# Performance work log

Measured on AMD Instinct MI355X. Metric: run time of the kernel, lower is better.

## Reference

```python
import jax, jax.numpy as jnp
import numpy as np

B, L, D, N, H = 4, 1024, 1024, 16, 64  # batch, seq, d_model, n_head, d_head
R = 2 * L  # relative position table length
EPS = 1e-5


def setup_inputs() -> dict:
    key = jax.random.key(0)
    ks = jax.random.split(key, 16)
    s = D ** -0.5
    q = jax.random.normal(ks[0], (B, L, D), jnp.float32)
    k = jax.random.normal(ks[1], (B, L, D), jnp.float32)
    v = jax.random.normal(ks[2], (B, L, D), jnp.float32)
    pos_encodings = jax.random.normal(ks[3], (R, D), jnp.float32)
    padding = jax.random.randint(ks[4], (B, 1, 1, L), 0, 2).astype(bool)
    q_w = jax.random.normal(ks[5], (D, N, H), jnp.float32) * s
    k_w = jax.random.normal(ks[6], (D, N, H), jnp.float32) * s
    k_b = jnp.zeros((N, H), jnp.float32)
    v_w = jax.random.normal(ks[7], (D, N, H), jnp.float32) * s
    v_b = jnp.zeros((N, H), jnp.float32)
    r_w_bias = jax.random.normal(ks[8], (N, 1, H), jnp.float32) * 0.02
    r_r_bias = jax.random.normal(ks[9], (N, 1, H), jnp.float32) * 0.02
    r_kernel = jax.random.normal(ks[10], (N, D, H), jnp.float32) * s
    post_w = jax.random.normal(ks[11], (N, H, D), jnp.float32) * (N * H) ** -0.5
    post_b = jnp.zeros((D,), jnp.float32)
    ln_g = jnp.ones((D,), jnp.float32)
    ln_b = jnp.zeros((D,), jnp.float32)
    return dict(q=q, k=k, v=v, pos_encodings=pos_encodings, padding=padding,
                q_w=q_w, k_w=k_w, k_b=k_b, v_w=v_w, v_b=v_b,
                r_w_bias=r_w_bias, r_r_bias=r_r_bias, r_kernel=r_kernel,
                post_w=post_w, post_b=post_b, ln_g=ln_g, ln_b=ln_b)


def _funnel_attention(q, k, v, pos_encodings, padding, q_w, k_w, k_b, v_w, v_b,
                      r_w_bias, r_r_bias, r_kernel, post_w, post_b, ln_g, ln_b):
    input_q = q
    d_head = q_w.shape[-1]
    scale = d_head ** -0.5
    # head projections, laid out [b, n, l, h]
    qh = jnp.einsum('bld,dnh->bnlh', q, q_w)
    kh = jnp.einsum('bld,dnh->bnlh', k, k_w) + k_b[None, :, None, :]
    vh = jnp.einsum('bld,dnh->bnlh', v, v_w) + v_b[None, :, None, :]
    # content term with r_w_bias
    attn_score = jnp.einsum('bnlh,bnmh->bnlm', qh + r_w_bias[None], kh) * scale
    # relative-position term (rel_shift)
    r = jnp.einsum('rd,ndh->nrh', pos_encodings, r_kernel)  # [n, R, h]
    pos = jnp.einsum('bnlh,nrh->bnlr', qh + r_r_bias[None], r) * scale  # [b,n,L,R]
    b, n, q_len, r_len = pos.shape
    k_len = kh.shape[-2]
    shift = 1 + (q_len != k_len)
    pos = pos.reshape(b, n, r_len, q_len)
    pos = pos[:, :, shift:, :]
    pos = pos.reshape(b, n, q_len, r_len - shift)[..., :k_len]
    attn_score = attn_score + pos
    # key padding mask
    attn_score = attn_score - 1e6 * padding.astype(attn_score.dtype)
    attn_dist = jax.nn.softmax(attn_score, axis=-1)
    out = jnp.einsum('bnlm,bnmh->bnlh', attn_dist, vh)
    attn_out = jnp.einsum('bnlh,nhd->bld', out, post_w) + post_b
    x = input_q + attn_out
    mu = jnp.mean(x, axis=-1, keepdims=True)
    var = jnp.mean(jnp.square(x - mu), axis=-1, keepdims=True)
    return (x - mu) * jax.lax.rsqrt(var + EPS) * ln_g + ln_b


def reference(q, k, v, pos_encodings, padding, q_w, k_w, k_b, v_w, v_b,
              r_w_bias, r_r_bias, r_kernel, post_w, post_b, ln_g, ln_b):
    return _funnel_attention(q, k, v, pos_encodings, padding, q_w, k_w, k_b,
                             v_w, v_b, r_w_bias, r_r_bias, r_kernel,
                             post_w, post_b, ln_g, ln_b)
```

## Files before the change

kernel.cpp:

```cpp
#include <hip/hip_runtime.h>
#include <hip/hip_bf16.h>

#define Bb 4
#define Ls 1024
#define Dd 1024
#define Nn 16
#define Hh 64
#define Rr 2048

typedef __attribute__((ext_vector_type(8))) short short8;
typedef __attribute__((ext_vector_type(4))) short short4v;
typedef __attribute__((ext_vector_type(4))) float f32x4;

__device__ __forceinline__ float bf2f(short s) {
    union { unsigned u; float f; } c;
    c.u = ((unsigned)(unsigned short)s) << 16;
    return c.f;
}
__device__ __forceinline__ short f2bf(float f) {
    __hip_bfloat16 h = __float2bfloat16(f);
    return *reinterpret_cast<short*>(&h);
}

__device__ __forceinline__ void gld16(const void* g, void* l) {
    __builtin_amdgcn_global_load_lds(
        (const __attribute__((address_space(1))) unsigned int*)g,
        (__attribute__((address_space(3))) unsigned int*)l, 16, 0, 0);
}

struct CopyDesc {
    const float* src[4];
    short* dst[4];
    int n[4];
};

__global__ __launch_bounds__(256) void f2bf_multi(CopyDesc cd) {
    const int z = blockIdx.y;
    const int base = (blockIdx.x * 256 + threadIdx.x) * 8;
    if (base >= cd.n[z]) return;
    const float* s = cd.src[z] + base;
    const float4 a = *(const float4*)s;
    const float4 b = *(const float4*)(s + 4);
    short8 o;
    o[0] = f2bf(a.x); o[1] = f2bf(a.y); o[2] = f2bf(a.z); o[3] = f2bf(a.w);
    o[4] = f2bf(b.x); o[5] = f2bf(b.y); o[6] = f2bf(b.z); o[7] = f2bf(b.w);
    *(short8*)(cd.dst[z] + base) = o;
}

struct TransDesc {
    const float* src[4];
    short* dst[4];
};

__global__ __launch_bounds__(256) void transpose_all(
    TransDesc td, const float* __restrict__ rker, short* __restrict__ rkT)
{
    const int z = blockIdx.z;
    const float* in; short* out; int C, R;
    if (z < 4) {
        in = td.src[z]; out = td.dst[z]; C = 1024; R = 1024;
    } else {
        if (blockIdx.x != 0) return;
        in  = rker + (long)(z - 4) * 1024 * 64;
        out = rkT  + (long)(z - 4) * 64 * 1024;
        C = 64; R = 1024;
    }
    const int r0 = blockIdx.y * 64, c0 = blockIdx.x * 64;
    __shared__ float T[64][65];
    const int t = threadIdx.x;
    const int rr = t >> 4, c4 = (t & 15) * 4;
#pragma unroll
    for (int p = 0; p < 4; ++p) {
        const float4 v = *(const float4*)&in[(long)(r0 + p * 16 + rr) * C + c0 + c4];
        T[p * 16 + rr][c4 + 0] = v.x;
        T[p * 16 + rr][c4 + 1] = v.y;
        T[p * 16 + rr][c4 + 2] = v.z;
        T[p * 16 + rr][c4 + 3] = v.w;
    }
    __syncthreads();
#pragma unroll
    for (int p = 0; p < 4; ++p) {
        const int j = p * 16 + (t >> 4);
        const int d4 = (t & 15) * 4;
        short4v o;
#pragma unroll
        for (int u = 0; u < 4; ++u) o[u] = f2bf(T[d4 + u][j]);
        *(short4v*)&out[(long)(c0 + j) * R + r0 + d4] = o;
    }
}

__global__ __launch_bounds__(256) void gemm_bt(
    const short* __restrict__ A, int lda, long aStride,
    const short* __restrict__ Bt, int ldb, long bStride,
    const float* __restrict__ bias,
    const float* __restrict__ kb, const float* __restrict__ vb,
    const float* __restrict__ residual, int ldr,
    void* __restrict__ Cv, int ldc, long cStride, int out_bf16, int K, int y3cut)
{
    const int z = blockIdx.z;
    if (z == 3 && (int)blockIdx.y >= y3cut) return;
    A  += (long)z * aStride;
    Bt += (long)z * bStride;

    const int row0 = blockIdx.y * 128;
    const int col0 = blockIdx.x * 128;

    __shared__ short As[128 * 32];
    __shared__ short Bs[128 * 32];

    const int tid  = threadIdx.x;
    const int w    = tid >> 6;
    const int lane = tid & 63;
    const int quad = lane >> 4;
    const int ln16 = lane & 15;
    const int wr   = (w >> 1) * 64;
    const int wc   = (w & 1) * 64;

    f32x4 acc[4][4];
#pragma unroll
    for (int a = 0; a < 4; ++a)
#pragma unroll
        for (int b = 0; b < 4; ++b) acc[a][b] = (f32x4){0.f, 0.f, 0.f, 0.f};

    const int srow = w * 16 + (lane >> 2);
    const int scol = (lane & 3) * 8;
    const short* gA = A  + (long)(row0 + srow) * lda + scol;
    const short* gB = Bt + (long)(col0 + srow) * ldb + scol;
    short* lA0 = As + w * 512;
    short* lB0 = Bs + w * 512;

    for (int k0 = 0; k0 < K; k0 += 32) {
        __syncthreads();
        gld16(gA + k0,                  lA0);
        gld16(gA + k0 + (long)64 * lda, lA0 + 2048);
        gld16(gB + k0,                  lB0);
        gld16(gB + k0 + (long)64 * ldb, lB0 + 2048);
        __syncthreads();

        short8 af[4], bfr[4];
#pragma unroll
        for (int tm = 0; tm < 4; ++tm)
            af[tm] = *(const short8*)&As[(wr + tm * 16 + ln16) * 32 + quad * 8];
#pragma unroll
        for (int tn = 0; tn < 4; ++tn)
            bfr[tn] = *(const short8*)&Bs[(wc + tn * 16 + ln16) * 32 + quad * 8];
#pragma unroll
        for (int tm = 0; tm < 4; ++tm)
#pragma unroll
            for (int tn = 0; tn < 4; ++tn)
                acc[tm][tn] = __builtin_amdgcn_mfma_f32_16x16x32_bf16(
                    af[tm], bfr[tn], acc[tm][tn], 0, 0, 0);
    }

    const float* bz = bias;
    if (z == 1) bz = kb;
    else if (z == 2) bz = vb;

    float bv[4];
#pragma unroll
    for (int tn = 0; tn < 4; ++tn)
        bv[tn] = bz ? bz[col0 + wc + tn * 16 + ln16] : 0.f;

    short* Cb = (short*)Cv + (long)z * cStride;
    float* Cf = (float*)Cv + (long)z * cStride;
#pragma unroll
    for (int tm = 0; tm < 4; ++tm) {
#pragma unroll
        for (int r = 0; r < 4; ++r) {
            const long row = row0 + wr + tm * 16 + quad * 4 + r;
#pragma unroll
            for (int tn = 0; tn < 4; ++tn) {
                const int col = col0 + wc + tn * 16 + ln16;
                float val = acc[tm][tn][r] + bv[tn];
                if (residual) val += residual[row * (long)ldr + col];
                if (out_bf16) Cb[row * (long)ldc + col] = f2bf(val);
                else          Cf[row * (long)ldc + col] = val;
            }
        }
    }
}

#define SCALE_L2E 0.18033688f

__global__ __launch_bounds__(256, 2) void attn_mfma(
    const short* __restrict__ qh, const short* __restrict__ kh,
    const short* __restrict__ vh, const short* __restrict__ rS,
    const int* __restrict__ padding, const float* __restrict__ rwb,
    const float* __restrict__ rrb, short* __restrict__ ao)
{
    const int lt = blockIdx.x, n = blockIdx.y, b = blockIdx.z;
    const int l0 = lt * 128;
    const int tid  = threadIdx.x;
    const int w    = tid >> 6;
    const int lane = tid & 63;
    const int quad = lane >> 4;
    const int ln16 = lane & 15;
    const int qb   = w * 32;

    __shared__ __align__(16) short ks[64][72];
    __shared__ __align__(16) short vsT[64][72];
    __shared__ __align__(16) short psm[4][16][72];
    __shared__ float padsAll[Ls];

    for (int i = tid; i < Ls; i += 256) {
        const float mask = -1.0e6f * (float)padding[b * Ls + i];
        padsAll[i] = (mask - 16.0f) * 1.44269504f;
    }

    short8 qwf[2][2], qrf[2][2];
#pragma unroll
    for (int qt = 0; qt < 2; ++qt) {
        const long rowoff =
            ((long)(b * Ls + l0 + qb + qt * 16 + ln16)) * (Nn * Hh) + n * Hh;
#pragma unroll
        for (int c = 0; c < 2; ++c) {
            const int kb2 = c * 32 + quad * 8;
            short8 qv = *(const short8*)(qh + rowoff + kb2);
#pragma unroll
            for (int j = 0; j < 8; ++j) {
                float qf = bf2f(qv[j]);
                qwf[qt][c][j] = f2bf(qf + rwb[n * Hh + kb2 + j]);
                qrf[qt][c][j] = f2bf(qf + rrb[n * Hh + kb2 + j]);
            }
        }
    }

    float lsum[2][4];
    f32x4 accO[2][4];
#pragma unroll
    for (int qt = 0; qt < 2; ++qt)
#pragma unroll
        for (int r = 0; r < 4; ++r) {
            lsum[qt][r] = 0.f;
            accO[qt][r] = (f32x4){0.f, 0.f, 0.f, 0.f};
        }

    for (int mt = 0; mt < Ls / 64; ++mt) {
        const int m0 = mt * 64;
        __syncthreads();

#pragma unroll
        for (int p = 0; p < 2; ++p) {
            int idx = tid + p * 256;
            int r_ = idx >> 3, cq = (idx & 7) * 8;
            *(short8*)&ks[r_][cq] =
                *(const short8*)(kh + ((long)(b * Ls + m0 + r_)) * 1024 + n * 64 + cq);
        }
        {
            int kp = tid & 31, cq = (tid >> 5) * 8;
            const short* vp = vh + ((long)(b * Ls + m0 + 2 * kp)) * 1024 + n * 64 + cq;
            short8 va = *(const short8*)vp;
            short8 vb2 = *(const short8*)(vp + 1024);
#pragma unroll
            for (int u = 0; u < 8; ++u) {
                unsigned pk = ((unsigned)(unsigned short)va[u]) |
                              (((unsigned)(unsigned short)vb2[u]) << 16);
                *(unsigned*)&vsT[cq + u][2 * kp] = pk;
            }
        }
        __syncthreads();

        const int baseU = 993 + m0 - l0 - qb;
        short8 rfU[6][2];
#pragma unroll
        for (int s = 0; s < 6; ++s) {
            int row = baseU + s * 16 + ln16;
            row = row < 2047 ? row : 2047;
            const short* rp = rS + (long)row * 1024 + n * 64 + quad * 8;
            rfU[s][0] = *(const short8*)rp;
            rfU[s][1] = *(const short8*)(rp + 32);
        }

#pragma unroll
        for (int qt = 0; qt < 2; ++qt) {
            const int off = qt ? 0 : 1;

            f32x4 Sf[4];
#pragma unroll
            for (int t = 0; t < 4; ++t) {
                f32x4 c = (f32x4){0.f, 0.f, 0.f, 0.f};
#pragma unroll
                for (int c2 = 0; c2 < 2; ++c2) {
                    short8 kf = *(short8*)&ks[t * 16 + ln16][c2 * 32 + quad * 8];
                    c = __builtin_amdgcn_mfma_f32_16x16x32_bf16(qwf[qt][c2], kf, c, 0, 0, 0);
                }
                Sf[t] = c;
            }
            f32x4 Prf[5];
#pragma unroll
            for (int t = 0; t < 5; ++t) {
                f32x4 c = (f32x4){0.f, 0.f, 0.f, 0.f};
                c = __builtin_amdgcn_mfma_f32_16x16x32_bf16(qrf[qt][0], rfU[t + off][0], c, 0, 0, 0);
                c = __builtin_amdgcn_mfma_f32_16x16x32_bf16(qrf[qt][1], rfU[t + off][1], c, 0, 0, 0);
                Prf[t] = c;
            }
            const float mb0 = padsAll[m0 + ln16];
            const float mb1 = padsAll[m0 + 16 + ln16];
            const float mb2 = padsAll[m0 + 32 + ln16];
            const float mb3 = padsAll[m0 + 48 + ln16];
#pragma unroll
            for (int r = 0; r < 4; ++r) {
                const int row = quad * 4 + r;
                const int u = ln16 - row + 15;
                const int srcLane = (quad << 4) | (u & 15);
                const float s0 = __shfl(Prf[0][r], srcLane, 64);
                const float s1 = __shfl(Prf[1][r], srcLane, 64);
                const float s2 = __shfl(Prf[2][r], srcLane, 64);
                const float s3 = __shfl(Prf[3][r], srcLane, 64);
                const float s4 = __shfl(Prf[4][r], srcLane, 64);
                const bool hi = (u >= 16);
                const float p0 = __builtin_amdgcn_exp2f(
                    fmaf(Sf[0][r] + (hi ? s1 : s0), SCALE_L2E, mb0));
                const float p1 = __builtin_amdgcn_exp2f(
                    fmaf(Sf[1][r] + (hi ? s2 : s1), SCALE_L2E, mb1));
                const float p2 = __builtin_amdgcn_exp2f(
                    fmaf(Sf[2][r] + (hi ? s3 : s2), SCALE_L2E, mb2));
                const float p3 = __builtin_amdgcn_exp2f(
                    fmaf(Sf[3][r] + (hi ? s4 : s3), SCALE_L2E, mb3));
                lsum[qt][r] += (p0 + p1) + (p2 + p3);
                psm[w][row][ln16]      = f2bf(p0);
                psm[w][row][16 + ln16] = f2bf(p1);
                psm[w][row][32 + ln16] = f2bf(p2);
                psm[w][row][48 + ln16] = f2bf(p3);
            }

            short8 pA[2];
#pragma unroll
            for (int c2 = 0; c2 < 2; ++c2)
                pA[c2] = *(short8*)&psm[w][ln16][c2 * 32 + quad * 8];
#pragma unroll
            for (int t = 0; t < 4; ++t) {
                f32x4 c = accO[qt][t];
#pragma unroll
                for (int c2 = 0; c2 < 2; ++c2) {
                    short8 vf = *(short8*)&vsT[t * 16 + ln16][c2 * 32 + quad * 8];
                    c = __builtin_amdgcn_mfma_f32_16x16x32_bf16(pA[c2], vf, c, 0, 0, 0);
                }
                accO[qt][t] = c;
            }
        }
    }

#pragma unroll
    for (int qt = 0; qt < 2; ++qt) {
#pragma unroll
        for (int r = 0; r < 4; ++r) {
            float v = lsum[qt][r];
#pragma unroll
            for (int of = 1; of < 16; of <<= 1) v += __shfl_xor(v, of, 64);
            lsum[qt][r] = 1.f / v;
        }
#pragma unroll
        for (int t = 0; t < 4; ++t)
#pragma unroll
            for (int r = 0; r < 4; ++r)
                psm[w][quad * 4 + r][t * 16 + ln16] =
                    f2bf(accO[qt][t][r] * lsum[qt][(unsigned)r]);
#pragma unroll
        for (int p = 0; p < 2; ++p) {
            const int c = lane + p * 64;
            const int row = c >> 3, cq = (c & 7) * 8;
            const long grow = (long)(b * Ls + l0 + qb + qt * 16 + row);
            *(short8*)(ao + grow * 1024 + n * 64 + cq) = *(short8*)&psm[w][row][cq];
        }
    }
}

__global__ __launch_bounds__(256) void ln_kernel(
    float* x, const float* __restrict__ g, const float* __restrict__ bb)
{
    const int row = blockIdx.x;
    const int tid = threadIdx.x;
    float4 v = ((const float4*)(x + (long)row * Dd))[tid];
    float s  = v.x + v.y + v.z + v.w;
    float sq = v.x * v.x + v.y * v.y + v.z * v.z + v.w * v.w;
#pragma unroll
    for (int off = 32; off; off >>= 1) {
        s  += __shfl_down(s, off, 64);
        sq += __shfl_down(sq, off, 64);
    }
    __shared__ float ws_s[4], ws_q[4];
    __shared__ float s_mu, s_rstd;
    const int wave = tid >> 6, lane = tid & 63;
    if (lane == 0) { ws_s[wave] = s; ws_q[wave] = sq; }
    __syncthreads();
    if (tid == 0) {
        const float ts = ws_s[0] + ws_s[1] + ws_s[2] + ws_s[3];
        const float tq = ws_q[0] + ws_q[1] + ws_q[2] + ws_q[3];
        const float mu = ts / (float)Dd;
        const float var = tq / (float)Dd - mu * mu;
        s_mu = mu;
        s_rstd = rsqrtf(var + 1e-5f);
    }
    __syncthreads();
    const float mu = s_mu, rstd = s_rstd;
    const float4 gv = ((const float4*)g)[tid];
    const float4 bv = ((const float4*)bb)[tid];
    float4 o;
    o.x = (v.x - mu) * rstd * gv.x + bv.x;
    o.y = (v.y - mu) * rstd * gv.y + bv.y;
    o.z = (v.z - mu) * rstd * gv.z + bv.z;
    o.w = (v.w - mu) * rstd * gv.w + bv.w;
    ((float4*)(x + (long)row * Dd))[tid] = o;
}

extern "C" void kernel_launch(void* const* d_in, const int* in_sizes, int n_in,
                              void* d_out, int out_size, void* d_ws, size_t ws_size,
                              hipStream_t stream) {
    const float* q      = (const float*)d_in[0];
    const float* k      = (const float*)d_in[1];
    const float* v      = (const float*)d_in[2];
    const float* posenc = (const float*)d_in[3];
    const int*   pad    = (const int*)  d_in[4];
    const float* q_w    = (const float*)d_in[5];
    const float* k_w    = (const float*)d_in[6];
    const float* k_b    = (const float*)d_in[7];
    const float* v_w    = (const float*)d_in[8];
    const float* v_b    = (const float*)d_in[9];
    const float* rwb    = (const float*)d_in[10];
    const float* rrb    = (const float*)d_in[11];
    const float* r_ker  = (const float*)d_in[12];
    const float* post_w = (const float*)d_in[13];
    const float* post_b = (const float*)d_in[14];
    const float* ln_g   = (const float*)d_in[15];
    const float* ln_b   = (const float*)d_in[16];
    float* out = (float*)d_out;

    const long M1 = 1L << 20;
    short* ws = (short*)d_ws;
    short* xq   = ws;
    short* xk   = ws + 4 * M1;
    short* xv   = ws + 8 * M1;
    short* pe   = ws + 12 * M1;
    short* wT   = ws + 14 * M1;
    short* rkT  = ws + 17 * M1;
    short* pwT  = ws + 18 * M1;
    short* qh   = ws + 19 * M1;
    short* kh   = ws + 23 * M1;
    short* vh   = ws + 27 * M1;
    short* rS   = ws + 31 * M1;
    short* ao   = xq;

    const dim3 blk(256);

    CopyDesc cd;
    cd.src[0] = q;      cd.dst[0] = xq;  cd.n[0] = 4 * (int)M1;
    cd.src[1] = k;      cd.dst[1] = xk;  cd.n[1] = 4 * (int)M1;
    cd.src[2] = v;      cd.dst[2] = xv;  cd.n[2] = 4 * (int)M1;
    cd.src[3] = posenc; cd.dst[3] = pe;  cd.n[3] = 2 * (int)M1;
    f2bf_multi<<<dim3(2048, 4), blk, 0, stream>>>(cd);

    TransDesc td;
    td.src[0] = q_w;    td.dst[0] = wT;
    td.src[1] = k_w;    td.dst[1] = wT + M1;
    td.src[2] = v_w;    td.dst[2] = wT + 2 * M1;
    td.src[3] = post_w; td.dst[3] = pwT;
    transpose_all<<<dim3(16, 16, 20), blk, 0, stream>>>(td, r_ker, rkT);

    gemm_bt<<<dim3(8, 32, 4), blk, 0, stream>>>(
        xq, 1024, 4 * M1, wT, 1024, M1, nullptr, k_b, v_b,
        nullptr, 0, qh, 1024, 4 * M1, 1, 1024, 16);

    attn_mfma<<<dim3(Ls / 128, Nn, Bb), blk, 0, stream>>>(
        qh, kh, vh, rS, pad, rwb, rrb, ao);

    gemm_bt<<<dim3(8, 32, 1), blk, 0, stream>>>(
        ao, 1024, 0, pwT, 1024, 0, post_b, nullptr, nullptr,
        q, 1024, out, 1024, 0, 0, 1024, 9999);

    ln_kernel<<<dim3(Bb * Ls), blk, 0, stream>>>(out, ln_g, ln_b);
}
```

Before: 333.9 us.

## Use 8 waves per attention block with one 16-row query tile each

```diff
diff --git a/kernel.cpp b/kernel.cpp
--- a/kernel.cpp
+++ b/kernel.cpp
@@ -182,7 +182,7 @@
 
 #define SCALE_L2E 0.18033688f
 
-__global__ __launch_bounds__(256, 2) void attn_mfma(
+__global__ __launch_bounds__(512, 4) void attn_mfma(
     const short* __restrict__ qh, const short* __restrict__ kh,
     const short* __restrict__ vh, const short* __restrict__ rS,
     const int* __restrict__ padding, const float* __restrict__ rwb,
@@ -195,23 +195,22 @@
     const int lane = tid & 63;
     const int quad = lane >> 4;
     const int ln16 = lane & 15;
-    const int qb   = w * 32;
+    const int qb   = w * 16;
 
     __shared__ __align__(16) short ks[64][72];
     __shared__ __align__(16) short vsT[64][72];
-    __shared__ __align__(16) short psm[4][16][72];
+    __shared__ __align__(16) short psm[8][16][72];
     __shared__ float padsAll[Ls];
 
-    for (int i = tid; i < Ls; i += 256) {
+    for (int i = tid; i < Ls; i += 512) {
         const float mask = -1.0e6f * (float)padding[b * Ls + i];
         padsAll[i] = (mask - 16.0f) * 1.44269504f;
     }
 
-    short8 qwf[2][2], qrf[2][2];
-#pragma unroll
-    for (int qt = 0; qt < 2; ++qt) {
+    short8 qwf[2], qrf[2];
+    {
         const long rowoff =
-            ((long)(b * Ls + l0 + qb + qt * 16 + ln16)) * (Nn * Hh) + n * Hh;
+            ((long)(b * Ls + l0 + qb + ln16)) * (Nn * Hh) + n * Hh;
 #pragma unroll
         for (int c = 0; c < 2; ++c) {
             const int kb2 = c * 32 + quad * 8;
@@ -219,150 +218,138 @@
 #pragma unroll
             for (int j = 0; j < 8; ++j) {
                 float qf = bf2f(qv[j]);
-                qwf[qt][c][j] = f2bf(qf + rwb[n * Hh + kb2 + j]);
-                qrf[qt][c][j] = f2bf(qf + rrb[n * Hh + kb2 + j]);
+                qwf[c][j] = f2bf(qf + rwb[n * Hh + kb2 + j]);
+                qrf[c][j] = f2bf(qf + rrb[n * Hh + kb2 + j]);
             }
         }
     }
 
-    float lsum[2][4];
-    f32x4 accO[2][4];
-#pragma unroll
-    for (int qt = 0; qt < 2; ++qt)
-#pragma unroll
-        for (int r = 0; r < 4; ++r) {
-            lsum[qt][r] = 0.f;
-            accO[qt][r] = (f32x4){0.f, 0.f, 0.f, 0.f};
-        }
+    float lsum[4];
+    f32x4 accO[4];
+#pragma unroll
+    for (int r = 0; r < 4; ++r) {
+        lsum[r] = 0.f;
+        accO[r] = (f32x4){0.f, 0.f, 0.f, 0.f};
+    }
 
     for (int mt = 0; mt < Ls / 64; ++mt) {
         const int m0 = mt * 64;
         __syncthreads();
 
-#pragma unroll
-        for (int p = 0; p < 2; ++p) {
-            int idx = tid + p * 256;
-            int r_ = idx >> 3, cq = (idx & 7) * 8;
+        {
+            const int r_ = tid >> 3, cq = (tid & 7) * 8;
             *(short8*)&ks[r_][cq] =
                 *(const short8*)(kh + ((long)(b * Ls + m0 + r_)) * 1024 + n * 64 + cq);
         }
         {
-            int kp = tid & 31, cq = (tid >> 5) * 8;
-            const short* vp = vh + ((long)(b * Ls + m0 + 2 * kp)) * 1024 + n * 64 + cq;
-            short8 va = *(const short8*)vp;
-            short8 vb2 = *(const short8*)(vp + 1024);
-#pragma unroll
-            for (int u = 0; u < 8; ++u) {
+            const int kp = tid & 31, c4 = (tid >> 5) * 4;
+            const short* vp = vh + ((long)(b * Ls + m0 + 2 * kp)) * 1024 + n * 64 + c4;
+            short4v va = *(const short4v*)vp;
+            short4v vb2 = *(const short4v*)(vp + 1024);
+#pragma unroll
+            for (int u = 0; u < 4; ++u) {
                 unsigned pk = ((unsigned)(unsigned short)va[u]) |
                               (((unsigned)(unsigned short)vb2[u]) << 16);
-                *(unsigned*)&vsT[cq + u][2 * kp] = pk;
+                *(unsigned*)&vsT[c4 + u][2 * kp] = pk;
             }
         }
         __syncthreads();
 
-        const int baseU = 993 + m0 - l0 - qb;
-        short8 rfU[6][2];
-#pragma unroll
-        for (int s = 0; s < 6; ++s) {
-            int row = baseU + s * 16 + ln16;
+        const int base5 = 1009 + m0 - l0 - qb;
+        short8 rfU[5][2];
+#pragma unroll
+        for (int s = 0; s < 5; ++s) {
+            int row = base5 + s * 16 + ln16;
             row = row < 2047 ? row : 2047;
             const short* rp = rS + (long)row * 1024 + n * 64 + quad * 8;
             rfU[s][0] = *(const short8*)rp;
             rfU[s][1] = *(const short8*)(rp + 32);
         }
 
-#pragma unroll
-        for (int qt = 0; qt < 2; ++qt) {
-            const int off = qt ? 0 : 1;
-
-            f32x4 Sf[4];
-#pragma unroll
-            for (int t = 0; t < 4; ++t) {
-                f32x4 c = (f32x4){0.f, 0.f, 0.f, 0.f};
-#pragma unroll
-                for (int c2 = 0; c2 < 2; ++c2) {
-                    short8 kf = *(short8*)&ks[t * 16 + ln16][c2 * 32 + quad * 8];
-                    c = __builtin_amdgcn_mfma_f32_16x16x32_bf16(qwf[qt][c2], kf, c, 0, 0, 0);
-                }
-                Sf[t] = c;
+        f32x4 Sf[4];
+#pragma unroll
+        for (int t = 0; t < 4; ++t) {
+            f32x4 c = (f32x4){0.f, 0.f, 0.f, 0.f};
+#pragma unroll
+            for (int c2 = 0; c2 < 2; ++c2) {
+                short8 kf = *(short8*)&ks[t * 16 + ln16][c2 * 32 + quad * 8];
+                c = __builtin_amdgcn_mfma_f32_16x16x32_bf16(qwf[c2], kf, c, 0, 0, 0);
             }
-            f32x4 Prf[5];
-#pragma unroll
-            for (int t = 0; t < 5; ++t) {
-                f32x4 c = (f32x4){0.f, 0.f, 0.f, 0.f};
-                c = __builtin_amdgcn_mfma_f32_16x16x32_bf16(qrf[qt][0], rfU[t + off][0], c, 0, 0, 0);
-                c = __builtin_amdgcn_mfma_f32_16x16x32_bf16(qrf[qt][1], rfU[t + off][1], c, 0, 0, 0);
-                Prf[t] = c;
+            Sf[t] = c;
+        }
+        f32x4 Prf[5];
+#pragma unroll
+        for (int t = 0; t < 5; ++t) {
+            f32x4 c = (f32x4){0.f, 0.f, 0.f, 0.f};
+            c = __builtin_amdgcn_mfma_f32_16x16x32_bf16(qrf[0], rfU[t][0], c, 0, 0, 0);
+            c = __builtin_amdgcn_mfma_f32_16x16x32_bf16(qrf[1], rfU[t][1], c, 0, 0, 0);
+            Prf[t] = c;
+        }
+        const float mb0 = padsAll[m0 + ln16];
+        const float mb1 = padsAll[m0 + 16 + ln16];
+        const float mb2 = padsAll[m0 + 32 + ln16];
+        const float mb3 = padsAll[m0 + 48 + ln16];
+#pragma unroll
+        for (int r = 0; r < 4; ++r) {
+            const int row = quad * 4 + r;
+            const int u = ln16 - row + 15;
+            const int srcLane = (quad << 4) | (u & 15);
+            const float s0 = __shfl(Prf[0][r], srcLane, 64);
+            const float s1 = __shfl(Prf[1][r], srcLane, 64);
+            const float s2 = __shfl(Prf[2][r], srcLane, 64);
+            const float s3 = __shfl(Prf[3][r], srcLane, 64);
+            const float s4 = __shfl(Prf[4][r], srcLane, 64);
+            const bool hi = (u >= 16);
+            const float p0 = __builtin_amdgcn_exp2f(
+                fmaf(Sf[0][r] + (hi ? s1 : s0), SCALE_L2E, mb0));
+            const float p1 = __builtin_amdgcn_exp2f(
+                fmaf(Sf[1][r] + (hi ? s2 : s1), SCALE_L2E, mb1));
+            const float p2 = __builtin_amdgcn_exp2f(
+                fmaf(Sf[2][r] + (hi ? s3 : s2), SCALE_L2E, mb2));
+            const float p3 = __builtin_amdgcn_exp2f(
+                fmaf(Sf[3][r] + (hi ? s4 : s3), SCALE_L2E, mb3));
+            lsum[r] += (p0 + p1) + (p2 + p3);
+            psm[w][row][ln16]      = f2bf(p0);
+            psm[w][row][16 + ln16] = f2bf(p1);
+            psm[w][row][32 + ln16] = f2bf(p2);
+            psm[w][row][48 + ln16] = f2bf(p3);
+        }
+
+        short8 pA[2];
+#pragma unroll
+        for (int c2 = 0; c2 < 2; ++c2)
+            pA[c2] = *(short8*)&psm[w][ln16][c2 * 32 + quad * 8];
+#pragma unroll
+        for (int t = 0; t < 4; ++t) {
+            f32x4 c = accO[t];
+#pragma unroll
+            for (int c2 = 0; c2 < 2; ++c2) {
+                short8 vf = *(short8*)&vsT[t * 16 + ln16][c2 * 32 + quad * 8];
+                c = __builtin_amdgcn_mfma_f32_16x16x32_bf16(pA[c2], vf, c, 0, 0, 0);
             }
-            const float mb0 = padsAll[m0 + ln16];
-            const float mb1 = padsAll[m0 + 16 + ln16];
-            const float mb2 = padsAll[m0 + 32 + ln16];
-            const float mb3 = padsAll[m0 + 48 + ln16];
-#pragma unroll
-            for (int r = 0; r < 4; ++r) {
-                const int row = quad * 4 + r;
-                const int u = ln16 - row + 15;
-                const int srcLane = (quad << 4) | (u & 15);
-                const float s0 = __shfl(Prf[0][r], srcLane, 64);
-                const float s1 = __shfl(Prf[1][r], srcLane, 64);
-                const float s2 = __shfl(Prf[2][r], srcLane, 64);
-                const float s3 = __shfl(Prf[3][r], srcLane, 64);
-                const float s4 = __shfl(Prf[4][r], srcLane, 64);
-                const bool hi = (u >= 16);
-                const float p0 = __builtin_amdgcn_exp2f(
-                    fmaf(Sf[0][r] + (hi ? s1 : s0), SCALE_L2E, mb0));
-                const float p1 = __builtin_amdgcn_exp2f(
-                    fmaf(Sf[1][r] + (hi ? s2 : s1), SCALE_L2E, mb1));
-                const float p2 = __builtin_amdgcn_exp2f(
-                    fmaf(Sf[2][r] + (hi ? s3 : s2), SCALE_L2E, mb2));
-                const float p3 = __builtin_amdgcn_exp2f(
-                    fmaf(Sf[3][r] + (hi ? s4 : s3), SCALE_L2E, mb3));
-                lsum[qt][r] += (p0 + p1) + (p2 + p3);
-                psm[w][row][ln16]      = f2bf(p0);
-                psm[w][row][16 + ln16] = f2bf(p1);
-                psm[w][row][32 + ln16] = f2bf(p2);
-                psm[w][row][48 + ln16] = f2bf(p3);
-            }
-
-            short8 pA[2];
-#pragma unroll
-            for (int c2 = 0; c2 < 2; ++c2)
-                pA[c2] = *(short8*)&psm[w][ln16][c2 * 32 + quad * 8];
-#pragma unroll
-            for (int t = 0; t < 4; ++t) {
-                f32x4 c = accO[qt][t];
-#pragma unroll
-                for (int c2 = 0; c2 < 2; ++c2) {
-                    short8 vf = *(short8*)&vsT[t * 16 + ln16][c2 * 32 + quad * 8];
-                    c = __builtin_amdgcn_mfma_f32_16x16x32_bf16(pA[c2], vf, c, 0, 0, 0);
-                }
-                accO[qt][t] = c;
-            }
-        }
-    }
-
-#pragma unroll
-    for (int qt = 0; qt < 2; ++qt) {
-#pragma unroll
-        for (int r = 0; r < 4; ++r) {
-            float v = lsum[qt][r];
-#pragma unroll
-            for (int of = 1; of < 16; of <<= 1) v += __shfl_xor(v, of, 64);
-            lsum[qt][r] = 1.f / v;
-        }
-#pragma unroll
-        for (int t = 0; t < 4; ++t)
-#pragma unroll
-            for (int r = 0; r < 4; ++r)
-                psm[w][quad * 4 + r][t * 16 + ln16] =
-                    f2bf(accO[qt][t][r] * lsum[qt][(unsigned)r]);
-#pragma unroll
-        for (int p = 0; p < 2; ++p) {
-            const int c = lane + p * 64;
-            const int row = c >> 3, cq = (c & 7) * 8;
-            const long grow = (long)(b * Ls + l0 + qb + qt * 16 + row);
-            *(short8*)(ao + grow * 1024 + n * 64 + cq) = *(short8*)&psm[w][row][cq];
-        }
+            accO[t] = c;
+        }
+    }
+
+#pragma unroll
+    for (int r = 0; r < 4; ++r) {
+        float v = lsum[r];
+#pragma unroll
+        for (int of = 1; of < 16; of <<= 1) v += __shfl_xor(v, of, 64);
+        lsum[r] = 1.f / v;
+    }
+#pragma unroll
+    for (int t = 0; t < 4; ++t)
+#pragma unroll
+        for (int r = 0; r < 4; ++r)
+            psm[w][quad * 4 + r][t * 16 + ln16] =
+                f2bf(accO[t][r] * lsum[(unsigned)r]);
+#pragma unroll
+    for (int p = 0; p < 2; ++p) {
+        const int c = lane + p * 64;
+        const int row = c >> 3, cq = (c & 7) * 8;
+        const long grow = (long)(b * Ls + l0 + qb + row);
+        *(short8*)(ao + grow * 1024 + n * 64 + cq) = *(short8*)&psm[w][row][cq];
     }
 }
 
@@ -461,7 +448,7 @@
         xq, 1024, 4 * M1, wT, 1024, M1, nullptr, k_b, v_b,
         nullptr, 0, qh, 1024, 4 * M1, 1, 1024, 16);
 
-    attn_mfma<<<dim3(Ls / 128, Nn, Bb), blk, 0, stream>>>(
+    attn_mfma<<<dim3(Ls / 128, Nn, Bb), dim3(512), 0, stream>>>(
         qh, kh, vh, rS, pad, rwb, rrb, ao);
 
     gemm_bt<<<dim3(8, 32, 1), blk, 0, stream>>>(
```

Result: slower. 366.2 us (+9.7%).

## Stage K and relative-position rows via async LDS loads with XOR swizzle, prefetch V

Applied to the files above, without the earlier changes.

```diff
diff --git a/kernel.cpp b/kernel.cpp
--- a/kernel.cpp
+++ b/kernel.cpp
@@ -197,7 +197,8 @@
     const int ln16 = lane & 15;
     const int qb   = w * 32;
 
-    __shared__ __align__(16) short ks[64][72];
+    __shared__ __align__(16) short ks[64 * 64];
+    __shared__ __align__(16) short rsb[192 * 64];
     __shared__ __align__(16) short vsT[64][72];
     __shared__ __align__(16) short psm[4][16][72];
     __shared__ float padsAll[Ls];
@@ -235,40 +236,64 @@
             accO[qt][r] = (f32x4){0.f, 0.f, 0.f, 0.f};
         }
 
+    const int srow8 = lane >> 3;
+    const int sunit = (lane & 7) ^ srow8;
+    const int swz   = ln16 & 7;
+
+    const int kp = tid & 31, cq = (tid >> 5) * 8;
+    short8 va, vb2;
+    {
+        const short* vp = vh + ((long)(b * Ls + 2 * kp)) * 1024 + n * 64 + cq;
+        va  = *(const short8*)vp;
+        vb2 = *(const short8*)(vp + 1024);
+    }
+
     for (int mt = 0; mt < Ls / 64; ++mt) {
         const int m0 = mt * 64;
         __syncthreads();
 
 #pragma unroll
-        for (int p = 0; p < 2; ++p) {
-            int idx = tid + p * 256;
-            int r_ = idx >> 3, cq = (idx & 7) * 8;
-            *(short8*)&ks[r_][cq] =
-                *(const short8*)(kh + ((long)(b * Ls + m0 + r_)) * 1024 + n * 64 + cq);
+        for (int j = 0; j < 2; ++j) {
+            const int c = w * 2 + j;
+            gld16(kh + ((long)(b * Ls + m0 + c * 8 + srow8)) * 1024
+                     + n * 64 + sunit * 8,
+                  ks + c * 512);
         }
         {
-            int kp = tid & 31, cq = (tid >> 5) * 8;
-            const short* vp = vh + ((long)(b * Ls + m0 + 2 * kp)) * 1024 + n * 64 + cq;
-            short8 va = *(const short8*)vp;
-            short8 vb2 = *(const short8*)(vp + 1024);
-#pragma unroll
-            for (int u = 0; u < 8; ++u) {
-                unsigned pk = ((unsigned)(unsigned short)va[u]) |
-                              (((unsigned)(unsigned short)vb2[u]) << 16);
-                *(unsigned*)&vsT[cq + u][2 * kp] = pk;
-            }
+            const int blockBase = 897 + m0 - l0;
+#pragma unroll
+            for (int j = 0; j < 6; ++j) {
+                const int c = w * 6 + j;
+                int rg = blockBase + c * 8 + srow8;
+                rg = rg < 2047 ? rg : 2047;
+                gld16(rS + (long)rg * 1024 + n * 64 + sunit * 8,
+                      rsb + c * 512);
+            }
+        }
+#pragma unroll
+        for (int u = 0; u < 8; ++u) {
+            unsigned pk = ((unsigned)(unsigned short)va[u]) |
+                          (((unsigned)(unsigned short)vb2[u]) << 16);
+            *(unsigned*)&vsT[cq + u][2 * kp] = pk;
         }
         __syncthreads();
 
-        const int baseU = 993 + m0 - l0 - qb;
+        {
+            const int mn = (m0 + 64) & (Ls - 1);
+            const short* vp = vh + ((long)(b * Ls + mn + 2 * kp)) * 1024 + n * 64 + cq;
+            va  = *(const short8*)vp;
+            vb2 = *(const short8*)(vp + 1024);
+        }
+
+        const int Rbase = (96 - qb) + ln16;
         short8 rfU[6][2];
 #pragma unroll
         for (int s = 0; s < 6; ++s) {
-            int row = baseU + s * 16 + ln16;
-            row = row < 2047 ? row : 2047;
-            const short* rp = rS + (long)row * 1024 + n * 64 + quad * 8;
-            rfU[s][0] = *(const short8*)rp;
-            rfU[s][1] = *(const short8*)(rp + 32);
+#pragma unroll
+            for (int c2 = 0; c2 < 2; ++c2) {
+                const int unit = (c2 * 4 + quad) ^ swz;
+                rfU[s][c2] = *(const short8*)&rsb[(Rbase + s * 16) * 64 + unit * 8];
+            }
         }
 
 #pragma unroll
@@ -281,7 +306,8 @@
                 f32x4 c = (f32x4){0.f, 0.f, 0.f, 0.f};
 #pragma unroll
                 for (int c2 = 0; c2 < 2; ++c2) {
-                    short8 kf = *(short8*)&ks[t * 16 + ln16][c2 * 32 + quad * 8];
+                    const int unit = (c2 * 4 + quad) ^ swz;
+                    short8 kf = *(const short8*)&ks[(t * 16 + ln16) * 64 + unit * 8];
                     c = __builtin_amdgcn_mfma_f32_16x16x32_bf16(qwf[qt][c2], kf, c, 0, 0, 0);
                 }
                 Sf[t] = c;
@@ -359,9 +385,9 @@
 #pragma unroll
         for (int p = 0; p < 2; ++p) {
             const int c = lane + p * 64;
-            const int row = c >> 3, cq = (c & 7) * 8;
+            const int row = c >> 3, cq2 = (c & 7) * 8;
             const long grow = (long)(b * Ls + l0 + qb + qt * 16 + row);
-            *(short8*)(ao + grow * 1024 + n * 64 + cq) = *(short8*)&psm[w][row][cq];
+            *(short8*)(ao + grow * 1024 + n * 64 + cq2) = *(short8*)&psm[w][row][cq2];
         }
     }
 }
```

Result: faster. 322.2 us (-3.5%).
